# Kernel tuning notes

Measured on AMD Instinct MI355X. Metric: run time of the kernel, lower is better.

The kernel has to match this reference:

```python
import jax, jax.numpy as jnp
import numpy as np
from jax import lax

B, Cin, H, W = 32, 11, 128, 128
K, P = 8, 7          # tile pitch, object size (7x7 solid rectangle per tile)
TN = H // K
ED, SD = 64, 32      # embed_dim, shape_embed_dim


def _conv(x, w, b, pad):
    y = lax.conv_general_dilated(x, w, (1, 1), [(pad, pad), (pad, pad)],
                                 dimension_numbers=('NCHW', 'OIHW', 'NCHW'))
    return y + b[None, :, None, None]


def _adaptive_maxpool_7_to_4(x):
    # torch AdaptiveMaxPool2d((4,4)) on 7x7: bins start=floor(i*7/4), end=ceil((i+1)*7/4)
    s, e = [0, 1, 3, 5], [2, 4, 6, 7]
    rows = jnp.stack([jnp.max(x[..., s[i]:e[i], :], axis=-2) for i in range(4)], axis=-2)
    return jnp.stack([jnp.max(rows[..., :, s[j]:e[j]], axis=-1) for j in range(4)], axis=-1)


def setup_inputs() -> dict:
    rng = np.random.default_rng(0)
    # tiled label grid: each KxK tile holds a PxP rectangle of a random class 1..10
    labels = rng.integers(1, Cin, (B, TN, TN))
    tile = np.zeros((K, K), dtype=np.int64); tile[:P, :P] = 1
    grid = (labels[:, :, None, :, None] * tile[None, None, :, None, :]).reshape(B, H, W)
    x = np.eye(Cin, dtype=np.float32)[grid].transpose(0, 3, 1, 2)  # (B,Cin,H,W) one-hot

    keys = jax.random.split(jax.random.key(0), 12)
    g = lambda k, sh: (jax.random.normal(k, sh, jnp.float32) * 0.05)
    return {
        'x': jnp.asarray(x),
        'conv1_w': g(keys[0], (ED, Cin, 3, 3)), 'conv1_b': g(keys[1], (ED,)),
        'conv2_w': g(keys[2], (ED, ED, 1, 1)), 'conv2_b': g(keys[3], (ED,)),
        'se_conv_w': g(keys[4], (16, 1, 3, 3)), 'se_conv_b': g(keys[5], (16,)),
        'se_lin_w': g(keys[6], (SD, 16 * 4 * 4)), 'se_lin_b': g(keys[7], (SD,)),
        'rp_w': g(keys[8], (SD, 2)), 'rp_b': g(keys[9], (SD,)),
        'fus_w': g(keys[10], (ED, ED + 2 * SD)), 'fus_b': g(keys[11], (ED,)),
    }


def reference(x, conv1_w, conv1_b, conv2_w, conv2_b, se_conv_w, se_conv_b,
              se_lin_w, se_lin_b, rp_w, rp_b, fus_w, fus_b):
    # pixel encoder: conv3x3 -> relu -> conv1x1
    pe = _conv(jax.nn.relu(_conv(x, conv1_w, conv1_b, 1)), conv2_w, conv2_b, 0)

    # every connected component is an identical PxP all-ones rectangle -> encode once
    mask = jnp.ones((1, 1, P, P), x.dtype)
    h = jax.nn.relu(_conv(mask, se_conv_w, se_conv_b, 1))            # (1,16,P,P)
    pooled = _adaptive_maxpool_7_to_4(h).reshape(1, -1)              # (1,256) C-major like torch Flatten
    shape_vec = jax.nn.relu(pooled @ se_lin_w.T + se_lin_b)[0]       # (SD,)

    yy, xx = jnp.meshgrid(jnp.linspace(0, 1, P), jnp.linspace(0, 1, P), indexing='ij')
    coords = jnp.stack([yy, xx], axis=-1).astype(x.dtype)            # (P,P,2)
    pos = (coords @ rp_w.T + rp_b).transpose(2, 0, 1)                # (SD,P,P)

    # scatter into dense maps: pattern per tile, tiled over the grid, masked by occupancy
    pat_s = jnp.zeros((SD, K, K), x.dtype).at[:, :P, :P].set(shape_vec[:, None, None])
    pat_p = jnp.zeros((SD, K, K), x.dtype).at[:, :P, :P].set(pos)
    occ = (jnp.argmax(x, axis=1) != 0).astype(x.dtype)               # (B,H,W)
    shape_map = jnp.tile(pat_s, (1, TN, TN))[None] * occ[:, None]    # (B,SD,H,W)
    rel_pos_map = jnp.tile(pat_p, (1, TN, TN))[None] * occ[:, None]
    shape_map = lax.stop_gradient(shape_map)
    rel_pos_map = lax.stop_gradient(rel_pos_map)

    combined = jnp.concatenate([pe, shape_map, rel_pos_map], axis=1).transpose(0, 2, 3, 1)
    fused = (combined @ fus_w.T + fus_b).transpose(0, 3, 1, 2)
    return pe + fused
```

## Files before the change

kernel.cpp:

```cpp
#include <hip/hip_runtime.h>
#include <hip/hip_bf16.h>

#define CIN 11


__device__ __forceinline__ unsigned short f2bfbits(float f) {
    union { float f; unsigned u; } cv; cv.f = f;
    unsigned u = cv.u;
    return (unsigned short)((u + 0x7FFFu + ((u >> 16) & 1u)) >> 16);
}

__device__ __forceinline__ float bfbits2f(unsigned s) {
    union { unsigned u; float f; } cv; cv.u = s << 16; return cv.f;
}

#define WS_W1T  0
#define WS_B1F  6336
#define WS_AT   6400
#define WS_DT   10496
#define WS_LM   14592
#define WS_TAB  16640
#define WS_FULL_BYTES 352384

__device__ __forceinline__ float direct_pixel(const float* __restrict__ ws,
                                              const unsigned char* lmb,
                                              float* dHrow,
                                              int h, int w, int l, float b1)
{
    float v = b1;
#pragma unroll
    for (int k = 0; k < 9; ++k) {
        int h2 = h + k / 3 - 1, w2 = w + k % 3 - 1;
        if (h2 >= 0 && h2 < 128 && w2 >= 0 && w2 < 128) {
            int i2 = h2 & 7, j2 = w2 & 7;
            int c = (i2 == 7 || j2 == 7) ? 0 : (int)lmb[(h2 >> 3) * 16 + (w2 >> 3)];
            v += ws[WS_W1T + (c * 9 + k) * 64 + l];
        }
    }
    dHrow[l] = fmaxf(v, 0.f);
    int ii = h & 7, j = w & 7;
    int didx = (ii < 7 && j < 7) ? (ii * 8 + j) : 63;
    float acc = ws[WS_DT + didx * 64 + l];
    const float4* hv4 = (const float4*)dHrow;
#pragma unroll
    for (int e4 = 0; e4 < 16; ++e4) {
        float4 hv = hv4[e4];
        acc += ws[WS_AT + (4 * e4 + 0) * 64 + l] * hv.x
             + ws[WS_AT + (4 * e4 + 1) * 64 + l] * hv.y
             + ws[WS_AT + (4 * e4 + 2) * 64 + l] * hv.z
             + ws[WS_AT + (4 * e4 + 3) * 64 + l] * hv.w;
    }
    return acc;
}

__global__ __launch_bounds__(256) void k1(
    const float* __restrict__ x,
    const float* __restrict__ c1w, const float* __restrict__ c1b,
    const float* __restrict__ c2w, const float* __restrict__ c2b,
    const float* __restrict__ sew, const float* __restrict__ seb,
    const float* __restrict__ selw, const float* __restrict__ selb,
    const float* __restrict__ rpw, const float* __restrict__ rpb,
    const float* __restrict__ fusw, const float* __restrict__ fusb,
    float* __restrict__ ws)
{
    const int t = threadIdx.x, blk = blockIdx.x;

    if (blk < 32) {
        int tt = blk * 256 + t;
        int b = tt >> 8, ty = (tt >> 4) & 15, tx = tt & 15;
        int h0 = ty * 8, w0 = tx * 8;
        int L = 0;
#pragma unroll
        for (int c = 0; c < CIN; ++c) {
            float v = x[((b * CIN + c) * 128 + h0) * 128 + w0];
            if (v > 0.5f) L = c;
        }
        ((unsigned char*)(ws + WS_LM))[tt] = (unsigned char)L;
    } else if (blk < 48) {
        int idx = (blk - 32) * 256 + t;
        int o = idx >> 6, e = idx & 63;
        float acc = c2w[o * 64 + e];
#pragma unroll 8
        for (int m = 0; m < 64; ++m)
            acc += fusw[o * 128 + m] * c2w[m * 64 + e];
        ws[WS_AT + e * 64 + o] = acc;
    } else if (blk < 64) {
        __shared__ float sh_hse[16 * 49];
        __shared__ float sh_pool[256];
        __shared__ float red[256];
        __shared__ float sh_sv[32];
        for (int idx = t; idx < 16 * 49; idx += 256) {
            int c = idx / 49, r = idx % 49, i = r / 7, j = r % 7;
            float a = seb[c];
            for (int di = 0; di < 3; ++di)
                for (int dj = 0; dj < 3; ++dj) {
                    int ri = i + di - 1, rj = j + dj - 1;
                    if (ri >= 0 && ri < 7 && rj >= 0 && rj < 7)
                        a += sew[c * 9 + di * 3 + dj];
                }
            sh_hse[idx] = fmaxf(a, 0.f);
        }
        __syncthreads();
        const int bs[4] = {0, 1, 3, 5}, be[4] = {2, 4, 6, 7};
        {
            int c = t >> 4, bi = (t >> 2) & 3, bj = t & 3;
            float m = -1e30f;
            for (int i = bs[bi]; i < be[bi]; ++i)
                for (int j = bs[bj]; j < be[bj]; ++j)
                    m = fmaxf(m, sh_hse[c * 49 + i * 7 + j]);
            sh_pool[t] = m;
        }
        __syncthreads();
        {
            int s = t >> 3, c8 = t & 7;
            float a = 0.f;
#pragma unroll 8
            for (int q = 0; q < 32; ++q)
                a += selw[s * 256 + c8 * 32 + q] * sh_pool[c8 * 32 + q];
            red[t] = a;
        }
        __syncthreads();
        if (t < 32) {
            float a = selb[t];
#pragma unroll
            for (int q = 0; q < 8; ++q) a += red[t * 8 + q];
            sh_sv[t] = fmaxf(a, 0.f);
        }
        __syncthreads();
        int idx = (blk - 48) * 256 + t;
        int o = idx >> 6, pi = idx & 63;
        int i = pi >> 3, j = pi & 7;
        float v = c2b[o] + fusb[o];
#pragma unroll 8
        for (int m = 0; m < 64; ++m)
            v += fusw[o * 128 + m] * c2b[m];
        if (i < 7 && j < 7) {
            float fi = i * (1.f / 6.f), fj = j * (1.f / 6.f);
#pragma unroll 4
            for (int s = 0; s < 32; ++s) {
                v += fusw[o * 128 + 64 + s] * sh_sv[s];
                float ps = rpw[2 * s] * fi + rpw[2 * s + 1] * fj + rpb[s];
                v += fusw[o * 128 + 96 + s] * ps;
            }
        }
        ws[WS_DT + pi * 64 + o] = v;
    } else {
        for (int idx = t; idx < CIN * 9 * 64; idx += 256) {
            int e = idx & 63, ck = idx >> 6, c = ck / 9, k = ck % 9;
            ws[WS_W1T + idx] = c1w[(e * CIN + c) * 9 + k];
        }
        if (t < 64) ws[WS_B1F + t] = c1b[t];
    }
}

__global__ __launch_bounds__(64) void k3(float* __restrict__ ws)
{
    const int id = blockIdx.x, l = threadIdx.x;
    unsigned short* TAB = (unsigned short*)(ws + WS_TAB);
    __shared__ float sh[64];

    int ctap[9];
    int didx = 63;
    if (id < 539) {
        int c = id / 49, r = id % 49, i = r / 7, j = r % 7;
        if (c != 0) didx = i * 8 + j;
        for (int k = 0; k < 9; ++k) {
            int ri = i + k / 3 - 1, rj = j + k % 3 - 1;
            ctap[k] = (ri >= 0 && ri < 7 && rj >= 0 && rj < 7) ? c : 0;
        }
    } else if (id < 1386) {
        int q = id - 539;
        int j = q / 121, lc = (q % 121) / 11, dc = q % 11;
        for (int k = 0; k < 9; ++k) {
            int di = k / 3, rj = j + k % 3 - 1;
            bool in7 = (rj >= 0 && rj < 7);
            ctap[k] = (di == 0) ? (in7 ? lc : 0) : (di == 1) ? 0 : (in7 ? dc : 0);
        }
    } else {
        int q = id - 1386;
        int i = q / 121, lc = (q % 121) / 11, rc = q % 11;
        for (int k = 0; k < 9; ++k) {
            int dj = k % 3, ri = i + k / 3 - 1;
            bool in7 = (ri >= 0 && ri < 7);
            ctap[k] = (dj == 0) ? (in7 ? lc : 0) : (dj == 1) ? 0 : (in7 ? rc : 0);
        }
    }
    float v = ws[WS_B1F + l];
#pragma unroll
    for (int k = 0; k < 9; ++k) v += ws[WS_W1T + (ctap[k] * 9 + k) * 64 + l];
    sh[l] = fmaxf(v, 0.f);
    __syncthreads();
    float acc = ws[WS_DT + didx * 64 + l];
    const float4* hv4 = (const float4*)sh;
#pragma unroll
    for (int e4 = 0; e4 < 16; ++e4) {
        float4 hv = hv4[e4];
        acc += ws[WS_AT + (4 * e4 + 0) * 64 + l] * hv.x
             + ws[WS_AT + (4 * e4 + 1) * 64 + l] * hv.y
             + ws[WS_AT + (4 * e4 + 2) * 64 + l] * hv.z
             + ws[WS_AT + (4 * e4 + 3) * 64 + l] * hv.w;
    }
    TAB[id * 64 + l] = f2bfbits(acc);
}

__global__ __launch_bounds__(256) void k4(const float* __restrict__ ws,
                                          float* __restrict__ out)
{
    const int b = blockIdx.x >> 7, h = blockIdx.x & 127;
    if (h == 0 || h == 127) return;

    const unsigned* LMg32 = (const unsigned*)(ws + WS_LM);
    const char* TABB = (const char*)(ws + WS_TAB);
    const int t = threadIdx.x;

    __shared__ float dHb[4][64];
    __shared__ unsigned cfg[128];
    __shared__ unsigned char dlist[128];
    __shared__ int dcnt;
    __shared__ unsigned char lmb[256];
    __shared__ __align__(16) unsigned short rowbuf[128 * 66];

    if (t < 64) ((unsigned*)lmb)[t] = LMg32[b * 64 + t];
    if (t == 0) dcnt = 0;
    __syncthreads();

    const int ii = h & 7, ty = h >> 3;

    if (t < 128) {
        int w = t, j = w & 7, tx = w >> 3;
        bool direct = (w == 0) | (w == 127) | (ii == 7 && j == 7);
        if (direct) {
            int p = atomicAdd(&dcnt, 1);
            dlist[p] = (unsigned char)w;
            cfg[w] = 0xFFFFFFFFu;
        } else {
            int L = lmb[ty * 16 + tx];
            int id;
            if (ii < 7 && j < 7) id = L * 49 + ii * 7 + j;
            else if (ii == 7)    id = 539 + j * 121 + L * 11 + (int)lmb[(ty + 1) * 16 + tx];
            else                 id = 1386 + ii * 121 + L * 11 + (int)lmb[ty * 16 + tx + 1];
            cfg[w] = (unsigned)(id * 64);
        }
    }
    __syncthreads();

    const int n = dcnt;
    const int g = t >> 6, l = t & 63;
    const float b1 = ws[WS_B1F + l];
    const int rounds = (n + 3) >> 2;
    for (int r = 0; r < rounds; ++r) {
        int di_ = r * 4 + g;
        if (di_ < n) {
            int w = (int)dlist[di_];
            float acc = direct_pixel(ws, lmb, dHb[g], h, w, l, b1);
            rowbuf[w * 66 + l] = f2bfbits(acc);
        }
    }

    {
        unsigned* rb32 = (unsigned*)rowbuf;
        int wA = (t >> 3), gg = t & 7;
        uint4 vv[4];
        unsigned cc[4];
#pragma unroll
        for (int p = 0; p < 4; ++p) {
            cc[p] = cfg[p * 32 + wA];
            unsigned c = (cc[p] == 0xFFFFFFFFu) ? 0u : cc[p];
            vv[p] = *(const uint4*)(TABB + (size_t)c * 2 + gg * 16);
        }
#pragma unroll
        for (int p = 0; p < 4; ++p) {
            if (cc[p] != 0xFFFFFFFFu) {
                int base = (p * 32 + wA) * 33 + gg * 4;
                rb32[base + 0] = vv[p].x; rb32[base + 1] = vv[p].y;
                rb32[base + 2] = vv[p].z; rb32[base + 3] = vv[p].w;
            }
        }
    }
    __syncthreads();

    {
        int wl = t & 63, th = t >> 6;
        for (int r = 0; r < 16; ++r) {
            int o = th * 16 + r;
            float* dst = out + ((size_t)(b * 64 + o) * 16384 + h * 128);
            dst[wl]      = bfbits2f(rowbuf[wl * 66 + o]);
            dst[wl + 64] = bfbits2f(rowbuf[(wl + 64) * 66 + o]);
        }
    }
}

__global__ __launch_bounds__(256) void k4b(const float* __restrict__ ws,
                                           float* __restrict__ out)
{
    const unsigned* LMg32 = (const unsigned*)(ws + WS_LM);
    const int bi = blockIdx.x;
    const int rI = bi >> 3;
    const int b = rI >> 1, h = (rI & 1) ? 127 : 0;
    const int w0 = (bi & 7) * 16;
    const int t = threadIdx.x, g = t >> 6, l = t & 63;

    __shared__ unsigned char lmb[256];
    __shared__ float dHb[4][64];
    __shared__ float sm[16][65];

    if (t < 64) ((unsigned*)lmb)[t] = LMg32[b * 64 + t];
    __syncthreads();

    const float b1 = ws[WS_B1F + l];
    for (int rr = 0; rr < 4; ++rr) {
        int p = rr * 4 + g;
        int w = w0 + p;
        sm[p][l] = direct_pixel(ws, lmb, dHb[g], h, w, l, b1);
    }
    __syncthreads();

#pragma unroll
    for (int q = 0; q < 4; ++q) {
        int idx = q * 256 + t;
        int o = idx >> 4, wq = idx & 15;
        out[(size_t)(b * 64 + o) * 16384 + h * 128 + w0 + wq] = sm[wq][o];
    }
}

__global__ __launch_bounds__(256) void k4d(const float* __restrict__ ws,
                                           float* __restrict__ out)
{
    const unsigned* LMg32 = (const unsigned*)(ws + WS_LM);
    const int t = threadIdx.x;
    const int b = blockIdx.x >> 7, h = blockIdx.x & 127;
    const int g = t >> 6, l = t & 63;

    __shared__ unsigned char lmb[256];
    __shared__ float dHb[4][64];
    __shared__ __align__(16) unsigned short rowbuf[128 * 66];

    if (t < 64) ((unsigned*)lmb)[t] = LMg32[b * 64 + t];
    __syncthreads();

    const float b1 = ws[WS_B1F + l];
    for (int r = 0; r < 32; ++r) {
        int w = r * 4 + g;
        float acc = direct_pixel(ws, lmb, dHb[g], h, w, l, b1);
        rowbuf[w * 66 + l] = f2bfbits(acc);
    }
    __syncthreads();
    {
        int wl = t & 63, th = t >> 6;
        for (int r = 0; r < 16; ++r) {
            int o = th * 16 + r;
            float* dst = out + ((size_t)(b * 64 + o) * 16384 + h * 128);
            dst[wl]      = bfbits2f(rowbuf[wl * 66 + o]);
            dst[wl + 64] = bfbits2f(rowbuf[(wl + 64) * 66 + o]);
        }
    }
}

extern "C" void kernel_launch(void* const* d_in, const int* in_sizes, int n_in,
                              void* d_out, int out_size, void* d_ws, size_t ws_size,
                              hipStream_t stream)
{
    (void)in_sizes; (void)n_in; (void)out_size;
    float* ws = (float*)d_ws;
    float* out = (float*)d_out;
    const int full = (ws_size >= (size_t)WS_FULL_BYTES) ? 1 : 0;

    hipLaunchKernelGGL(k1, dim3(65), dim3(256), 0, stream,
                       (const float*)d_in[0], (const float*)d_in[1], (const float*)d_in[2],
                       (const float*)d_in[3], (const float*)d_in[4], (const float*)d_in[5],
                       (const float*)d_in[6], (const float*)d_in[7], (const float*)d_in[8],
                       (const float*)d_in[9], (const float*)d_in[10], (const float*)d_in[11],
                       (const float*)d_in[12], ws);
    if (full) {
        hipLaunchKernelGGL(k3, dim3(2233), dim3(64), 0, stream, ws);
        hipLaunchKernelGGL(k4, dim3(4096), dim3(256), 0, stream, ws, out);
        hipLaunchKernelGGL(k4b, dim3(512), dim3(256), 0, stream, ws, out);
    } else {
        hipLaunchKernelGGL(k4d, dim3(4096), dim3(256), 0, stream, ws, out);
    }
}
```

Measured before the change: 261.4 us.

## Split row kernel into table-gather writer and separate sparse direct-pixel kernel

Replaces the per-row kernel, which mixed direct conv evaluation for border and tile-corner pixels with table lookups, by a pure table-gather kernel. Each thread in that kernel owns one output column and streams all 64 channels straight to global memory with no shared-memory staging. The remaining direct pixels (left/right image columns and tile corners) move to a new kernel k4c that spreads them evenly across blocks, so row blocks no longer serialise on a few expensive pixels. The cost is an extra launch and scattered single-element stores in k4c. The gather kernel may also overwrite corner pixels with a dummy entry before k4c runs.

```diff
diff --git a/kernel.cpp b/kernel.cpp
--- a/kernel.cpp
+++ b/kernel.cpp
@@ -203,82 +203,122 @@
     TAB[id * 64 + l] = f2bfbits(acc);
 }
 
-__global__ __launch_bounds__(256) void k4(const float* __restrict__ ws,
-                                          float* __restrict__ out)
-{
+__global__ __launch_bounds__(256) void k4m(const float* __restrict__ ws,
+                                           float* __restrict__ out)
+{
+    const int bi = blockIdx.x;
+    const int b = bi >> 5, ty = (bi >> 1) & 15, half = bi & 1;
+    const int t = threadIdx.x, g = t >> 6, l = t & 63;
+    const char* TABB = (const char*)(ws + WS_TAB);
+
+    __shared__ unsigned char lmb[256];
+    if (t < 64) ((unsigned*)lmb)[t] = ((const unsigned*)(ws + WS_LM))[b * 64 + t];
+    __syncthreads();
+
+    const int w = half * 64 + l;
+    const int tx = w >> 3, j = w & 7;
+    const int L  = lmb[ty * 16 + tx];
+    const int Lr = lmb[ty * 16 + (tx < 15 ? tx + 1 : 15)];
+    const int Ld = lmb[(ty < 15 ? ty + 1 : 15) * 16 + tx];
+
+#pragma unroll
+    for (int rr = 0; rr < 2; ++rr) {
+        const int ii = g * 2 + rr;
+        const int h = ty * 8 + ii;
+        int id;
+        if (ii < 7) id = (j < 7) ? (L * 49 + ii * 7 + j) : (1386 + ii * 121 + L * 11 + Lr);
+        else        id = (j < 7) ? (539 + j * 121 + L * 11 + Ld) : 0;
+        const char* src = TABB + (size_t)id * 128;
+        float* dst = out + ((size_t)b * 64 * 16384 + h * 128 + w);
+#pragma unroll 8
+        for (int o = 0; o < 64; o += 2) {
+            unsigned u = *(const unsigned*)(src + 2 * o);
+            dst[(size_t)(o)     * 16384] = bfbits2f(u & 0xFFFFu);
+            dst[(size_t)(o + 1) * 16384] = bfbits2f(u >> 16);
+        }
+    }
+}
+
+__global__ __launch_bounds__(256) void k4b(const float* __restrict__ ws,
+                                           float* __restrict__ out)
+{
+    const unsigned* LMg32 = (const unsigned*)(ws + WS_LM);
+    const int bi = blockIdx.x;
+    const int rI = bi >> 3;
+    const int b = rI >> 1, h = (rI & 1) ? 127 : 0;
+    const int w0 = (bi & 7) * 16;
+    const int t = threadIdx.x, g = t >> 6, l = t & 63;
+
+    __shared__ unsigned char lmb[256];
+    __shared__ float dHb[4][64];
+    __shared__ float sm[16][65];
+
+    if (t < 64) ((unsigned*)lmb)[t] = LMg32[b * 64 + t];
+    __syncthreads();
+
+    const float b1 = ws[WS_B1F + l];
+    for (int rr = 0; rr < 4; ++rr) {
+        int p = rr * 4 + g;
+        sm[p][l] = direct_pixel(ws, lmb, dHb[g], h, w0 + p, l, b1);
+    }
+    __syncthreads();
+
+#pragma unroll
+    for (int q = 0; q < 4; ++q) {
+        int idx = q * 256 + t;
+        int o = idx >> 4, wq = idx & 15;
+        out[(size_t)(b * 64 + o) * 16384 + h * 128 + w0 + wq] = sm[wq][o];
+    }
+}
+
+__global__ __launch_bounds__(256) void k4c(const float* __restrict__ ws,
+                                           float* __restrict__ out)
+{
+    const unsigned* LMg32 = (const unsigned*)(ws + WS_LM);
+    const int t = threadIdx.x, g = t >> 6, l = t & 63;
+
+    __shared__ unsigned char lmb4[4][256];
+    __shared__ float dHb[4][64];
+
+    const float b1 = ws[WS_B1F + l];
+    for (int rr = 0; rr < 4; ++rr) {
+        int idx = blockIdx.x * 16 + rr * 4 + g;
+        int b, h, w;
+        if (idx < 8064) {
+            int q = idx; b = q / 252; int r = q - b * 252;
+            h = 1 + (r >> 1); w = (r & 1) ? 127 : 0;
+        } else {
+            int q = idx - 8064; b = q / 225; int r = q - b * 225;
+            h = 7 + 8 * (r / 15); w = 7 + 8 * (r % 15);
+        }
+        ((unsigned*)lmb4[g])[l] = LMg32[b * 64 + l];
+        float acc = direct_pixel(ws, lmb4[g], dHb[g], h, w, l, b1);
+        out[(size_t)(b * 64 + l) * 16384 + h * 128 + w] = acc;
+    }
+}
+
+__global__ __launch_bounds__(256) void k4d(const float* __restrict__ ws,
+                                           float* __restrict__ out)
+{
+    const unsigned* LMg32 = (const unsigned*)(ws + WS_LM);
+    const int t = threadIdx.x;
     const int b = blockIdx.x >> 7, h = blockIdx.x & 127;
-    if (h == 0 || h == 127) return;
-
-    const unsigned* LMg32 = (const unsigned*)(ws + WS_LM);
-    const char* TABB = (const char*)(ws + WS_TAB);
-    const int t = threadIdx.x;
-
+    const int g = t >> 6, l = t & 63;
+
+    __shared__ unsigned char lmb[256];
     __shared__ float dHb[4][64];
-    __shared__ unsigned cfg[128];
-    __shared__ unsigned char dlist[128];
-    __shared__ int dcnt;
-    __shared__ unsigned char lmb[256];
     __shared__ __align__(16) unsigned short rowbuf[128 * 66];
 
     if (t < 64) ((unsigned*)lmb)[t] = LMg32[b * 64 + t];
-    if (t == 0) dcnt = 0;
-    __syncthreads();
-
-    const int ii = h & 7, ty = h >> 3;
-
-    if (t < 128) {
-        int w = t, j = w & 7, tx = w >> 3;
-        bool direct = (w == 0) | (w == 127) | (ii == 7 && j == 7);
-        if (direct) {
-            int p = atomicAdd(&dcnt, 1);
-            dlist[p] = (unsigned char)w;
-            cfg[w] = 0xFFFFFFFFu;
-        } else {
-            int L = lmb[ty * 16 + tx];
-            int id;
-            if (ii < 7 && j < 7) id = L * 49 + ii * 7 + j;
-            else if (ii == 7)    id = 539 + j * 121 + L * 11 + (int)lmb[(ty + 1) * 16 + tx];
-            else                 id = 1386 + ii * 121 + L * 11 + (int)lmb[ty * 16 + tx + 1];
-            cfg[w] = (unsigned)(id * 64);
-        }
-    }
-    __syncthreads();
-
-    const int n = dcnt;
-    const int g = t >> 6, l = t & 63;
+    __syncthreads();
+
     const float b1 = ws[WS_B1F + l];
-    const int rounds = (n + 3) >> 2;
-    for (int r = 0; r < rounds; ++r) {
-        int di_ = r * 4 + g;
-        if (di_ < n) {
-            int w = (int)dlist[di_];
-            float acc = direct_pixel(ws, lmb, dHb[g], h, w, l, b1);
-            rowbuf[w * 66 + l] = f2bfbits(acc);
-        }
-    }
-
-    {
-        unsigned* rb32 = (unsigned*)rowbuf;
-        int wA = (t >> 3), gg = t & 7;
-        uint4 vv[4];
-        unsigned cc[4];
-#pragma unroll
-        for (int p = 0; p < 4; ++p) {
-            cc[p] = cfg[p * 32 + wA];
-            unsigned c = (cc[p] == 0xFFFFFFFFu) ? 0u : cc[p];
-            vv[p] = *(const uint4*)(TABB + (size_t)c * 2 + gg * 16);
-        }
-#pragma unroll
-        for (int p = 0; p < 4; ++p) {
-            if (cc[p] != 0xFFFFFFFFu) {
-                int base = (p * 32 + wA) * 33 + gg * 4;
-                rb32[base + 0] = vv[p].x; rb32[base + 1] = vv[p].y;
-                rb32[base + 2] = vv[p].z; rb32[base + 3] = vv[p].w;
-            }
-        }
-    }
-    __syncthreads();
-
+    for (int r = 0; r < 32; ++r) {
+        int w = r * 4 + g;
+        float acc = direct_pixel(ws, lmb, dHb[g], h, w, l, b1);
+        rowbuf[w * 66 + l] = f2bfbits(acc);
+    }
+    __syncthreads();
     {
         int wl = t & 63, th = t >> 6;
         for (int r = 0; r < 16; ++r) {
@@ -290,72 +330,6 @@
     }
 }
 
-__global__ __launch_bounds__(256) void k4b(const float* __restrict__ ws,
-                                           float* __restrict__ out)
-{
-    const unsigned* LMg32 = (const unsigned*)(ws + WS_LM);
-    const int bi = blockIdx.x;
-    const int rI = bi >> 3;
-    const int b = rI >> 1, h = (rI & 1) ? 127 : 0;
-    const int w0 = (bi & 7) * 16;
-    const int t = threadIdx.x, g = t >> 6, l = t & 63;
-
-    __shared__ unsigned char lmb[256];
-    __shared__ float dHb[4][64];
-    __shared__ float sm[16][65];
-
-    if (t < 64) ((unsigned*)lmb)[t] = LMg32[b * 64 + t];
-    __syncthreads();
-
-    const float b1 = ws[WS_B1F + l];
-    for (int rr = 0; rr < 4; ++rr) {
-        int p = rr * 4 + g;
-        int w = w0 + p;
-        sm[p][l] = direct_pixel(ws, lmb, dHb[g], h, w, l, b1);
-    }
-    __syncthreads();
-
-#pragma unroll
-    for (int q = 0; q < 4; ++q) {
-        int idx = q * 256 + t;
-        int o = idx >> 4, wq = idx & 15;
-        out[(size_t)(b * 64 + o) * 16384 + h * 128 + w0 + wq] = sm[wq][o];
-    }
-}
-
-__global__ __launch_bounds__(256) void k4d(const float* __restrict__ ws,
-                                           float* __restrict__ out)
-{
-    const unsigned* LMg32 = (const unsigned*)(ws + WS_LM);
-    const int t = threadIdx.x;
-    const int b = blockIdx.x >> 7, h = blockIdx.x & 127;
-    const int g = t >> 6, l = t & 63;
-
-    __shared__ unsigned char lmb[256];
-    __shared__ float dHb[4][64];
-    __shared__ __align__(16) unsigned short rowbuf[128 * 66];
-
-    if (t < 64) ((unsigned*)lmb)[t] = LMg32[b * 64 + t];
-    __syncthreads();
-
-    const float b1 = ws[WS_B1F + l];
-    for (int r = 0; r < 32; ++r) {
-        int w = r * 4 + g;
-        float acc = direct_pixel(ws, lmb, dHb[g], h, w, l, b1);
-        rowbuf[w * 66 + l] = f2bfbits(acc);
-    }
-    __syncthreads();
-    {
-        int wl = t & 63, th = t >> 6;
-        for (int r = 0; r < 16; ++r) {
-            int o = th * 16 + r;
-            float* dst = out + ((size_t)(b * 64 + o) * 16384 + h * 128);
-            dst[wl]      = bfbits2f(rowbuf[wl * 66 + o]);
-            dst[wl + 64] = bfbits2f(rowbuf[(wl + 64) * 66 + o]);
-        }
-    }
-}
-
 extern "C" void kernel_launch(void* const* d_in, const int* in_sizes, int n_in,
                               void* d_out, int out_size, void* d_ws, size_t ws_size,
                               hipStream_t stream)
@@ -372,9 +346,10 @@
                        (const float*)d_in[9], (const float*)d_in[10], (const float*)d_in[11],
                        (const float*)d_in[12], ws);
     if (full) {
-        hipLaunchKernelGGL(k3, dim3(2233), dim3(64), 0, stream, ws);
-        hipLaunchKernelGGL(k4, dim3(4096), dim3(256), 0, stream, ws, out);
-        hipLaunchKernelGGL(k4b, dim3(512), dim3(256), 0, stream, ws, out);
+        hipLaunchKernelGGL(k3,  dim3(2233), dim3(256 / 4), 0, stream, ws);
+        hipLaunchKernelGGL(k4m, dim3(1024), dim3(256), 0, stream, ws, out);
+        hipLaunchKernelGGL(k4b, dim3(512),  dim3(256), 0, stream, ws, out);
+        hipLaunchKernelGGL(k4c, dim3(954),  dim3(256), 0, stream, ws, out);
     } else {
         hipLaunchKernelGGL(k4d, dim3(4096), dim3(256), 0, stream, ws, out);
     }
```

Result: faster. 209.7 us (-19.8%).
